# Performance work log

Measured on AMD Instinct MI355X. Metric: run time of the kernel, lower is better.

The kernel has to match this reference:

```python
import jax, jax.numpy as jnp
import numpy as np

GROUPS = 32  # min(32, 256//4)
EPS = 1e-5


def setup_inputs() -> dict:
    key = jax.random.key(0)
    ks = jax.random.split(key, 4)
    B, C, H, W = 8, 256, 128, 128
    x = jax.random.normal(ks[0], (B, C, H, W), dtype=jnp.float32)
    gn_w = jnp.ones((C,), dtype=jnp.float32)
    gn_b = jnp.zeros((C,), dtype=jnp.float32)
    qkv_w = jax.random.normal(ks[1], (3 * C, C), dtype=jnp.float32) * (C ** -0.5)
    qkv_b = jnp.zeros((3 * C,), dtype=jnp.float32)
    proj_w = jax.random.normal(ks[2], (C, C), dtype=jnp.float32) * (C ** -0.5)
    proj_b = jnp.zeros((C,), dtype=jnp.float32)
    return {"x": x, "gn_w": gn_w, "gn_b": gn_b, "qkv_w": qkv_w,
            "qkv_b": qkv_b, "proj_w": proj_w, "proj_b": proj_b}


def _group_norm(x, w, b):
    B, C, H, W = x.shape
    xg = x.reshape(B, GROUPS, C // GROUPS, H, W)
    mean = xg.mean(axis=(2, 3, 4), keepdims=True)
    var = xg.var(axis=(2, 3, 4), keepdims=True)
    xg = (xg - mean) * jax.lax.rsqrt(var + EPS)
    x = xg.reshape(B, C, H, W)
    return x * w[None, :, None, None] + b[None, :, None, None]


def reference(x, gn_w, gn_b, qkv_w, qkv_b, proj_w, proj_b):
    B, C, H, W = x.shape
    num_heads = 8
    head_dim = C // num_heads
    scale = head_dim ** -0.5

    h = _group_norm(x, gn_w, gn_b)
    # 1x1 conv == per-pixel matmul over channels
    qkv = jnp.einsum('bchw,oc->bohw', h, qkv_w) + qkv_b[None, :, None, None]
    qkv = qkv.reshape(B, 3, num_heads, head_dim, H * W)
    q, k, v = qkv[:, 0], qkv[:, 1], qkv[:, 2]  # each (B, h, head_dim, HW)
    # Faithful to source: contracts over spatial axis d=HW -> (B,h,hd,hd)
    attn = jnp.einsum('bhid,bhjd->bhij', q, k) * scale
    attn = jax.nn.softmax(attn, axis=-1)
    out = jnp.einsum('bhij,bhjd->bhid', attn, v)  # (B, h, head_dim, HW)
    out = out.reshape(B, C, H, W)
    out = jnp.einsum('bchw,oc->bohw', out, proj_w) + proj_b[None, :, None, None]
    return x + out
```

## Files before the change

### kernel.cpp

```cpp
#include <hip/hip_runtime.h>
#include <stdint.h>

typedef __bf16 bf16;
typedef __attribute__((ext_vector_type(8))) __bf16 bf16x8;
typedef __attribute__((ext_vector_type(4))) float f32x4;

#define S_HW 16384
#define N_C 256

__device__ __forceinline__ f32x4 mfma16(bf16x8 a, bf16x8 b, f32x4 c) {
  return __builtin_amdgcn_mfma_f32_16x16x32_bf16(a, b, c, 0, 0, 0);
}
__device__ __forceinline__ void async_ld16(const bf16* g, bf16* l) {
  __builtin_amdgcn_global_load_lds(
      (const __attribute__((address_space(1))) unsigned int*)g,
      (__attribute__((address_space(3))) unsigned int*)l, 16, 0, 0);
}
__device__ __forceinline__ unsigned short bf2u(bf16 h) {
  union { bf16 h; unsigned short u; } c; c.h = h; return c.u;
}
__device__ __forceinline__ bf16 u2bf(unsigned short u) {
  union { unsigned short u; bf16 h; } c; c.u = u; return c.h;
}

__global__ __launch_bounds__(256) void k_split(
    const float* __restrict__ x, bf16* __restrict__ yhi, bf16* __restrict__ ylo,
    bf16* __restrict__ yt, float* __restrict__ Sx) {
  int b = blockIdx.z, c0 = blockIdx.y * 64, s0 = blockIdx.x * 64;
  __shared__ unsigned T[64][65];
  __shared__ float sxl[256];
  int t = threadIdx.x;
  int cl = t >> 2, sg = t & 3;
  size_t off = (size_t)(b * N_C + c0 + cl) * S_HW + s0 + sg * 16;
  const float* xp = x + off;
  bf16x8 hv[2], lv[2];
  float sum = 0.f;
#pragma unroll
  for (int i2 = 0; i2 < 4; i2++) {
    float4 v = *(const float4*)(xp + i2 * 4);
    float f4[4] = {v.x, v.y, v.z, v.w};
#pragma unroll
    for (int k = 0; k < 4; k++) {
      int i = i2 * 4 + k;
      float fv = f4[k];
      bf16 h = (bf16)fv;
      bf16 l = (bf16)(fv - (float)h);
      hv[i >> 3][i & 7] = h;
      lv[i >> 3][i & 7] = l;
      sum += fv;
      T[sg * 16 + i][cl] = (unsigned)bf2u(h) | ((unsigned)bf2u(l) << 16);
    }
  }
  *(bf16x8*)(yhi + off) = hv[0];
  *(bf16x8*)(yhi + off + 8) = hv[1];
  *(bf16x8*)(ylo + off) = lv[0];
  *(bf16x8*)(ylo + off + 8) = lv[1];
  sxl[t] = sum;
  __syncthreads();
  if (t < 64) {
    float s2 = sxl[t * 4] + sxl[t * 4 + 1] + sxl[t * 4 + 2] + sxl[t * 4 + 3];
    atomicAdd(&Sx[b * N_C + c0 + t], s2);
  }
  int sl = t >> 2, cg = t & 3;
  bf16x8 ho[2], lo2[2];
#pragma unroll
  for (int i = 0; i < 16; i++) {
    unsigned u = T[sl][cg * 16 + i];
    ho[i >> 3][i & 7] = u2bf((unsigned short)(u & 0xffffu));
    lo2[i >> 3][i & 7] = u2bf((unsigned short)(u >> 16));
  }
  size_t tb = (size_t)(b * S_HW + s0 + sl) * 512 + c0 + cg * 16;
  *(bf16x8*)(yt + tb) = ho[0];
  *(bf16x8*)(yt + tb + 8) = ho[1];
  *(bf16x8*)(yt + tb + 256) = lo2[0];
  *(bf16x8*)(yt + tb + 256 + 8) = lo2[1];
}

__global__ __launch_bounds__(256) void k_gram(
    const bf16* __restrict__ yhi, const bf16* __restrict__ ylo,
    float* __restrict__ YG3) {
  constexpr int BK = 32;
  __shared__ __align__(16) bf16 As[128 * BK];
  __shared__ __align__(16) bf16 Bs[128 * BK];
  int kc = blockIdx.x * 2048;
  int m0 = (blockIdx.y >> 2) * 128, n0 = (blockIdx.y & 3) * 128;
  int b = blockIdx.z;
  int tid = threadIdx.x, lane = tid & 63, wave = tid >> 6;
  int wm = (wave >> 1) * 64, wn = (wave & 1) * 64;
  const bf16* Ab = yhi + (size_t)(b * N_C + m0) * S_HW;
  const bf16* Bb = (n0 < 256) ? yhi + (size_t)(b * N_C + n0) * S_HW
                              : ylo + (size_t)(b * N_C + n0 - 256) * S_HW;
  f32x4 acc[4][4] = {};
  for (int kt = kc; kt < kc + 2048; kt += BK) {
#pragma unroll
    for (int i = 0; i < 2; i++) {
      int ch = i * 256 + tid;
      int row = ch >> 2, col = (ch & 3) * 8;
      async_ld16(Ab + (size_t)row * S_HW + kt + col, As + (i * 256 + wave * 64) * 8);
      async_ld16(Bb + (size_t)row * S_HW + kt + col, Bs + (i * 256 + wave * 64) * 8);
    }
    __syncthreads();
    bf16x8 af[4], bfr[4];
    int fm = lane & 15, fk = (lane >> 4) * 8;
#pragma unroll
    for (int q = 0; q < 4; q++) {
      af[q] = *(const bf16x8*)(As + (wm + q * 16 + fm) * BK + fk);
      bfr[q] = *(const bf16x8*)(Bs + (wn + q * 16 + fm) * BK + fk);
    }
#pragma unroll
    for (int ti = 0; ti < 4; ti++)
#pragma unroll
      for (int tj = 0; tj < 4; tj++)
        acc[ti][tj] = mfma16(af[ti], bfr[tj], acc[ti][tj]);
    __syncthreads();
  }
  int quad = lane >> 4, cn = lane & 15;
#pragma unroll
  for (int ti = 0; ti < 4; ti++)
#pragma unroll
    for (int r = 0; r < 4; r++) {
      int m = m0 + wm + ti * 16 + quad * 4 + r;
#pragma unroll
      for (int tj = 0; tj < 4; tj++) {
        int n = n0 + wn + tj * 16 + cn;
        atomicAdd(&YG3[(size_t)(b * N_C + m) * 512 + n], acc[ti][tj][r]);
      }
    }
}

__global__ __launch_bounds__(256) void k_wkt(const float* __restrict__ qkv_w,
                                             float* __restrict__ WkT) {
  int k = blockIdx.x, j = threadIdx.x;
  WkT[k * 256 + j] = qkv_w[(256 + j) * 256 + k];
}

__global__ __launch_bounds__(256) void k_coefs(
    const float* __restrict__ Sx, const float* __restrict__ YG3,
    const float* __restrict__ gn_w, const float* __restrict__ gn_b,
    const float* __restrict__ qkv_w, const float* __restrict__ qkv_b,
    float* __restrict__ a_, float* __restrict__ bv_, float* __restrict__ u_,
    float* __restrict__ vbe) {
  int b = blockIdx.x, t = threadIdx.x;
  __shared__ float sxl[256], gxd[256], gm[32], gr[32], sh[256], bl[256];
  sxl[t] = Sx[b * N_C + t];
  gxd[t] = YG3[(size_t)(b * N_C + t) * 512 + t] +
           2.f * YG3[(size_t)(b * N_C + t) * 512 + 256 + t];
  __syncthreads();
  if (t < 32) {
    float s = 0.f, q2 = 0.f;
#pragma unroll
    for (int i = 0; i < 8; i++) { s += sxl[t * 8 + i]; q2 += gxd[t * 8 + i]; }
    float mean = s * (1.f / 131072.f);
    float var = q2 * (1.f / 131072.f) - mean * mean;
    gm[t] = mean;
    gr[t] = 1.f / sqrtf(var + 1e-5f);
  }
  __syncthreads();
  {
    float A = gn_w[t] * gr[t >> 3];
    float B = gn_b[t] - gm[t >> 3] * A;
    a_[b * N_C + t] = A;
    bv_[b * N_C + t] = B;
    bl[t] = B;
    sh[t] = A * sxl[t] + 16384.f * B;
  }
  __syncthreads();
  for (int r = t; r < 512; r += 256) {
    const float* wp = qkv_w + (size_t)r * 256;
    float acc = 0.f;
    for (int c = 0; c < 256; c++) acc += wp[c] * sh[c];
    u_[b * 512 + r] = acc;
  }
  {
    const float* wp = qkv_w + (size_t)(512 + t) * 256;
    float acc = 0.f;
    for (int c = 0; c < 256; c++) acc += wp[c] * bl[c];
    vbe[b * N_C + t] = acc + qkv_b[512 + t];
  }
}

__global__ __launch_bounds__(256) void k_t1(
    const float* __restrict__ YG3, const float* __restrict__ WkT,
    const float* __restrict__ a_, const float* __restrict__ bv_,
    const float* __restrict__ Sx, float* __restrict__ T1) {
  int tile = blockIdx.x, b = blockIdx.y;
  int i0 = (tile >> 2) * 64, j0 = (tile & 3) * 64;
  __shared__ float As[64][69];
  __shared__ float Bs[64][69];
  __shared__ float al[256], bl[256], sxl[256];
  int t = threadIdx.x;
  al[t] = a_[b * N_C + t];
  bl[t] = bv_[b * N_C + t];
  sxl[t] = Sx[b * N_C + t];
  int cl = t >> 2, qq = (t & 3) * 16;
  int kk = t >> 2, jj = (t & 3) * 16;
  int ti = t >> 4, tj = t & 15;
  float acc[4][4] = {};
  for (int kc = 0; kc < 256; kc += 64) {
    {
      const float* yg = YG3 + (size_t)(b * N_C + i0 + cl) * 512 + kc + qq;
#pragma unroll
      for (int i = 0; i < 16; i++) As[cl][qq + i] = yg[i] + yg[256 + i];
    }
    __syncthreads();
    {
      int cp = kc + kk;
      const float* ygp = YG3 + (size_t)(b * N_C + cp) * 512 + 256 + i0 + jj;
#pragma unroll
      for (int i = 0; i < 16; i++) As[jj + i][kk] += ygp[i];
    }
    __syncthreads();
    {
      int c = i0 + cl;
      float ac = al[c], bc = bl[c], sxc = sxl[c];
#pragma unroll
      for (int i = 0; i < 16; i++) {
        int cp = kc + qq + i;
        As[cl][qq + i] = ac * al[cp] * As[cl][qq + i] + ac * bl[cp] * sxc +
                         bc * al[cp] * sxl[cp] + 16384.f * bc * bl[cp];
      }
    }
    {
      const float* wp = WkT + (size_t)(kc + kk) * 256 + j0 + jj;
#pragma unroll
      for (int i = 0; i < 16; i += 4) {
        float4 v = *(const float4*)(wp + i);
        Bs[kk][jj + i] = v.x; Bs[kk][jj + i + 1] = v.y;
        Bs[kk][jj + i + 2] = v.z; Bs[kk][jj + i + 3] = v.w;
      }
    }
    __syncthreads();
    for (int k = 0; k < 64; k++) {
      float av[4], bv4[4];
#pragma unroll
      for (int ii = 0; ii < 4; ii++) av[ii] = As[ti * 4 + ii][k];
#pragma unroll
      for (int j2 = 0; j2 < 4; j2++) bv4[j2] = Bs[k][tj * 4 + j2];
#pragma unroll
      for (int ii = 0; ii < 4; ii++)
#pragma unroll
        for (int j2 = 0; j2 < 4; j2++) acc[ii][j2] += av[ii] * bv4[j2];
    }
    __syncthreads();
  }
#pragma unroll
  for (int ii = 0; ii < 4; ii++)
#pragma unroll
    for (int j2 = 0; j2 < 4; j2++)
      T1[(size_t)(b * N_C + i0 + ti * 4 + ii) * 256 + j0 + tj * 4 + j2] =
          acc[ii][j2];
}

__global__ __launch_bounds__(256) void k_logits(
    const float* __restrict__ T1, const float* __restrict__ qkv_w,
    const float* __restrict__ qkv_b, const float* __restrict__ u_,
    float* __restrict__ attn) {
  int h = blockIdx.x, b = blockIdx.y;
  __shared__ float Tc[64][33];
  __shared__ float Wql[32][65];
  __shared__ float Ll[32][33];
  __shared__ float uq[32], uk[32], bq[32], bk[32];
  int t = threadIdx.x;
  if (t < 32) {
    uq[t] = u_[b * 512 + h * 32 + t];
    uk[t] = u_[b * 512 + 256 + h * 32 + t];
    bq[t] = qkv_b[h * 32 + t];
    bk[t] = qkv_b[256 + h * 32 + t];
  }
  int i = t & 31, jg = t >> 5;
  float acc[4] = {};
  for (int cc = 0; cc < 256; cc += 64) {
    {
      int c_l = t >> 2, seg = (t & 3) * 8;
      const float* tp = T1 + (size_t)(b * N_C + cc + c_l) * 256 + h * 32 + seg;
      float4 v0 = *(const float4*)tp, v1 = *(const float4*)(tp + 4);
      Tc[c_l][seg] = v0.x; Tc[c_l][seg + 1] = v0.y;
      Tc[c_l][seg + 2] = v0.z; Tc[c_l][seg + 3] = v0.w;
      Tc[c_l][seg + 4] = v1.x; Tc[c_l][seg + 5] = v1.y;
      Tc[c_l][seg + 6] = v1.z; Tc[c_l][seg + 7] = v1.w;
      int row = t >> 3, seg2 = (t & 7) * 8;
      const float* wp = qkv_w + (size_t)(h * 32 + row) * 256 + cc + seg2;
      float4 w0 = *(const float4*)wp, w1 = *(const float4*)(wp + 4);
      Wql[row][seg2] = w0.x; Wql[row][seg2 + 1] = w0.y;
      Wql[row][seg2 + 2] = w0.z; Wql[row][seg2 + 3] = w0.w;
      Wql[row][seg2 + 4] = w1.x; Wql[row][seg2 + 5] = w1.y;
      Wql[row][seg2 + 6] = w1.z; Wql[row][seg2 + 7] = w1.w;
    }
    __syncthreads();
    for (int c = 0; c < 64; c++) {
      float w = Wql[i][c];
#pragma unroll
      for (int j2 = 0; j2 < 4; j2++) acc[j2] += w * Tc[c][jg * 4 + j2];
    }
    __syncthreads();
  }
  const float scale = 0.17677669529663687f;
#pragma unroll
  for (int j2 = 0; j2 < 4; j2++) {
    int j = jg * 4 + j2;
    Ll[i][j] = scale * (acc[j2] + bq[i] * uk[j] + bk[j] * uq[i] +
                        16384.f * bq[i] * bk[j]);
  }
  __syncthreads();
  if (t < 32) {
    float m = -1e30f;
    for (int j = 0; j < 32; j++) m = fmaxf(m, Ll[t][j]);
    float e[32], s = 0.f;
    for (int j = 0; j < 32; j++) { e[j] = expf(Ll[t][j] - m); s += e[j]; }
    float inv = 1.f / s;
    float* ap = attn + (size_t)((b * 8 + h) * 32 + t) * 32;
    for (int j = 0; j < 32; j++) ap[j] = e[j] * inv;
  }
}

__global__ __launch_bounds__(256) void k_m1(const float* __restrict__ proj_w,
                                            const float* __restrict__ attn,
                                            float* __restrict__ M1) {
  int o = blockIdx.x, b = blockIdx.y, t = threadIdx.x;
  __shared__ float at[8192];
  __shared__ float pl[256];
  for (int k = 0; k < 8192; k += 256) at[k + t] = attn[(size_t)b * 8192 + k + t];
  pl[t] = proj_w[(size_t)o * 256 + t];
  __syncthreads();
  int h = t >> 5, j = t & 31;
  float acc = 0.f;
#pragma unroll
  for (int i = 0; i < 32; i++) acc += pl[h * 32 + i] * at[h * 1024 + i * 32 + j];
  M1[(size_t)(b * N_C + o) * 256 + t] = acc;
}

__global__ __launch_bounds__(256) void k_m2(const float* __restrict__ M1,
                                            const float* __restrict__ qkv_w,
                                            float* __restrict__ M2) {
  int tile = blockIdx.x, b = blockIdx.y;
  int i0 = (tile >> 2) * 64, j0 = (tile & 3) * 64;
  __shared__ float As[64][69];
  __shared__ float Bs[64][69];
  int t = threadIdx.x;
  int cl = t >> 2, qq = (t & 3) * 16;
  int kk = t >> 2, jj = (t & 3) * 16;
  int ti = t >> 4, tj = t & 15;
  float acc[4][4] = {};
  for (int kc = 0; kc < 256; kc += 64) {
    {
      const float* mp = M1 + (size_t)(b * N_C + i0 + cl) * 256 + kc + qq;
#pragma unroll
      for (int i = 0; i < 16; i += 4) {
        float4 v = *(const float4*)(mp + i);
        As[cl][qq + i] = v.x; As[cl][qq + i + 1] = v.y;
        As[cl][qq + i + 2] = v.z; As[cl][qq + i + 3] = v.w;
      }
      const float* wp = qkv_w + (size_t)(512 + kc + kk) * 256 + j0 + jj;
#pragma unroll
      for (int i = 0; i < 16; i += 4) {
        float4 v = *(const float4*)(wp + i);
        Bs[kk][jj + i] = v.x; Bs[kk][jj + i + 1] = v.y;
        Bs[kk][jj + i + 2] = v.z; Bs[kk][jj + i + 3] = v.w;
      }
    }
    __syncthreads();
    for (int k = 0; k < 64; k++) {
      float av[4], bv4[4];
#pragma unroll
      for (int ii = 0; ii < 4; ii++) av[ii] = As[ti * 4 + ii][k];
#pragma unroll
      for (int j2 = 0; j2 < 4; j2++) bv4[j2] = Bs[k][tj * 4 + j2];
#pragma unroll
      for (int ii = 0; ii < 4; ii++)
#pragma unroll
        for (int j2 = 0; j2 < 4; j2++) acc[ii][j2] += av[ii] * bv4[j2];
    }
    __syncthreads();
  }
#pragma unroll
  for (int ii = 0; ii < 4; ii++)
#pragma unroll
    for (int j2 = 0; j2 < 4; j2++)
      M2[(size_t)(b * N_C + i0 + ti * 4 + ii) * 256 + j0 + tj * 4 + j2] =
          acc[ii][j2];
}

__global__ __launch_bounds__(256) void k_fa(
    const float* __restrict__ M2, const float* __restrict__ M1,
    const float* __restrict__ a_, const float* __restrict__ vbe,
    const float* __restrict__ proj_b, bf16* __restrict__ FA,
    float* __restrict__ g_) {
  int o = blockIdx.x, b = blockIdx.y, t = threadIdx.x;
  float f = M2[(size_t)(b * N_C + o) * 256 + t] * a_[b * N_C + t];
  bf16 hi = (bf16)f;
  bf16 lo = (bf16)(f - (float)hi);
  FA[(size_t)(b * N_C + o) * 512 + t] = hi;
  FA[(size_t)(b * N_C + o) * 512 + 256 + t] = lo;
  __shared__ float red[256];
  red[t] = M1[(size_t)(b * N_C + o) * 256 + t] * vbe[b * N_C + t];
  __syncthreads();
  for (int s2 = 128; s2 > 0; s2 >>= 1) {
    if (t < s2) red[t] += red[t + s2];
    __syncthreads();
  }
  if (t == 0) g_[b * N_C + o] = red[0] + proj_b[o];
}

__global__ __launch_bounds__(256) void k_final(
    const bf16* __restrict__ FA, const bf16* __restrict__ yt,
    const float* __restrict__ g_, const float* __restrict__ x,
    float* __restrict__ out) {
  constexpr int BK = 32;
  __shared__ __align__(16) bf16 As[128 * BK];
  __shared__ __align__(16) bf16 Bs[128 * BK];
  int b = blockIdx.z, m0 = blockIdx.y * 128, n0 = blockIdx.x * 128;
  int tid = threadIdx.x, lane = tid & 63, wave = tid >> 6;
  int wm = (wave >> 1) * 64, wn = (wave & 1) * 64;
  const bf16* Ab = FA + (size_t)(b * N_C + m0) * 512;
  const bf16* Bb = yt + (size_t)(b * S_HW + n0) * 512;
  f32x4 acc[4][4] = {};
  for (int kt = 0; kt < 768; kt += BK) {
    int ka = (kt < 512) ? kt : kt - 512;
    int kb = (kt < 256) ? kt : kt - 256;
#pragma unroll
    for (int i = 0; i < 2; i++) {
      int ch = i * 256 + tid;
      int row = ch >> 2, col = (ch & 3) * 8;
      async_ld16(Ab + (size_t)row * 512 + ka + col, As + (i * 256 + wave * 64) * 8);
      async_ld16(Bb + (size_t)row * 512 + kb + col, Bs + (i * 256 + wave * 64) * 8);
    }
    __syncthreads();
    bf16x8 af[4], bfr[4];
    int fm = lane & 15, fk = (lane >> 4) * 8;
#pragma unroll
    for (int q = 0; q < 4; q++) {
      af[q] = *(const bf16x8*)(As + (wm + q * 16 + fm) * BK + fk);
      bfr[q] = *(const bf16x8*)(Bs + (wn + q * 16 + fm) * BK + fk);
    }
#pragma unroll
    for (int ti = 0; ti < 4; ti++)
#pragma unroll
      for (int tj = 0; tj < 4; tj++)
        acc[ti][tj] = mfma16(af[ti], bfr[tj], acc[ti][tj]);
    __syncthreads();
  }
  int quad = lane >> 4, cn = lane & 15;
#pragma unroll
  for (int ti = 0; ti < 4; ti++)
#pragma unroll
    for (int r = 0; r < 4; r++) {
      int row = m0 + wm + ti * 16 + quad * 4 + r;
      float gb = g_[b * N_C + row];
#pragma unroll
      for (int tj = 0; tj < 4; tj++) {
        int col = n0 + wn + tj * 16 + cn;
        size_t idx = (size_t)(b * N_C + row) * S_HW + col;
        out[idx] = acc[ti][tj][r] + gb + x[idx];
      }
    }
}

extern "C" void kernel_launch(void* const* d_in, const int* in_sizes, int n_in,
                              void* d_out, int out_size, void* d_ws,
                              size_t ws_size, hipStream_t stream) {
  const float* x = (const float*)d_in[0];
  const float* gn_w = (const float*)d_in[1];
  const float* gn_b = (const float*)d_in[2];
  const float* qkv_w = (const float*)d_in[3];
  const float* qkv_b = (const float*)d_in[4];
  const float* proj_w = (const float*)d_in[5];
  const float* proj_b = (const float*)d_in[6];
  float* out = (float*)d_out;

  const size_t MB = 1ull << 20;
  char* ws = (char*)d_ws;
  bf16* ylo = (bf16*)ws;
  bf16* yt = (bf16*)(ws + 64 * MB);
  float* YG3 = (float*)(ws + 192 * MB);
  float* M1 = (float*)(ws + 192 * MB);
  bf16* FA = (bf16*)(ws + 194 * MB);
  float* WkT = (float*)(ws + 196 * MB);
  float* attn = (float*)(ws + 196 * MB + 256 * 1024);
  float* Sx = (float*)(ws + 196 * MB + 512 * 1024);
  float* a_ = (float*)(ws + 196 * MB + 520 * 1024);
  float* bv_ = (float*)(ws + 196 * MB + 528 * 1024);
  float* u_ = (float*)(ws + 196 * MB + 536 * 1024);
  float* vbe = (float*)(ws + 196 * MB + 552 * 1024);
  float* g_ = (float*)(ws + 196 * MB + 560 * 1024);
  float* T1 = (float*)(ws + 198 * MB);
  float* M2 = T1;
  bf16* yhi = (bf16*)d_out;

  if (ws_size < 200 * MB) return;

  hipMemsetAsync(YG3, 0, 4 * MB, stream);
  hipMemsetAsync(Sx, 0, 8 * 1024, stream);
  k_split<<<dim3(256, 4, 8), 256, 0, stream>>>(x, yhi, ylo, yt, Sx);
  k_gram<<<dim3(8, 8, 8), 256, 0, stream>>>(yhi, ylo, YG3);
  k_wkt<<<256, 256, 0, stream>>>(qkv_w, WkT);
  k_coefs<<<8, 256, 0, stream>>>(Sx, YG3, gn_w, gn_b, qkv_w, qkv_b, a_, bv_,
                                 u_, vbe);
  k_t1<<<dim3(16, 8), 256, 0, stream>>>(YG3, WkT, a_, bv_, Sx, T1);
  k_logits<<<dim3(8, 8), 256, 0, stream>>>(T1, qkv_w, qkv_b, u_, attn);
  k_m1<<<dim3(256, 8), 256, 0, stream>>>(proj_w, attn, M1);
  k_m2<<<dim3(16, 8), 256, 0, stream>>>(M1, qkv_w, M2);
  k_fa<<<dim3(256, 8), 256, 0, stream>>>(M2, M1, a_, vbe, proj_b, FA, g_);
  k_final<<<dim3(128, 2, 8), 256, 0, stream>>>(FA, yt, g_, x, out);
}
```

Before: 574.8 us.

## Fold residual into final GEMM via identity and double-buffer LDS tiles

The residual add x is folded into the final GEMM. k_fa adds 1.0 on the diagonal of FA, so the product with yt, which holds the bf16 hi/lo split of x, reproduces x. This drops the separate fp32 read of x in k_final's epilogue. Separately, k_gram and k_final get two LDS buffers per operand so the next K-tile is prefetched while the current one is consumed. The risks are slightly lower residual precision (a bf16 hi+lo reconstruction instead of exact fp32) and doubled LDS use per block, which may reduce occupancy.

```diff
diff --git a/kernel.cpp b/kernel.cpp
--- a/kernel.cpp
+++ b/kernel.cpp
@@ -80,8 +80,8 @@
     const bf16* __restrict__ yhi, const bf16* __restrict__ ylo,
     float* __restrict__ YG3) {
   constexpr int BK = 32;
-  __shared__ __align__(16) bf16 As[128 * BK];
-  __shared__ __align__(16) bf16 Bs[128 * BK];
+  __shared__ __align__(16) bf16 As[2][128 * BK];
+  __shared__ __align__(16) bf16 Bs[2][128 * BK];
   int kc = blockIdx.x * 2048;
   int m0 = (blockIdx.y >> 2) * 128, n0 = (blockIdx.y & 3) * 128;
   int b = blockIdx.z;
@@ -91,21 +91,30 @@
   const bf16* Bb = (n0 < 256) ? yhi + (size_t)(b * N_C + n0) * S_HW
                               : ylo + (size_t)(b * N_C + n0 - 256) * S_HW;
   f32x4 acc[4][4] = {};
-  for (int kt = kc; kt < kc + 2048; kt += BK) {
+
+  auto STAGE = [&](int buf, int kt) {
 #pragma unroll
     for (int i = 0; i < 2; i++) {
       int ch = i * 256 + tid;
       int row = ch >> 2, col = (ch & 3) * 8;
-      async_ld16(Ab + (size_t)row * S_HW + kt + col, As + (i * 256 + wave * 64) * 8);
-      async_ld16(Bb + (size_t)row * S_HW + kt + col, Bs + (i * 256 + wave * 64) * 8);
-    }
-    __syncthreads();
+      async_ld16(Ab + (size_t)row * S_HW + kt + col,
+                 &As[buf][(i * 256 + wave * 64) * 8]);
+      async_ld16(Bb + (size_t)row * S_HW + kt + col,
+                 &Bs[buf][(i * 256 + wave * 64) * 8]);
+    }
+  };
+
+  STAGE(0, kc);
+  __syncthreads();
+  int cur = 0;
+  for (int kt = kc; kt < kc + 2048; kt += BK) {
+    if (kt + BK < kc + 2048) STAGE(cur ^ 1, kt + BK);
     bf16x8 af[4], bfr[4];
     int fm = lane & 15, fk = (lane >> 4) * 8;
 #pragma unroll
     for (int q = 0; q < 4; q++) {
-      af[q] = *(const bf16x8*)(As + (wm + q * 16 + fm) * BK + fk);
-      bfr[q] = *(const bf16x8*)(Bs + (wn + q * 16 + fm) * BK + fk);
+      af[q] = *(const bf16x8*)(&As[cur][(wm + q * 16 + fm) * BK + fk]);
+      bfr[q] = *(const bf16x8*)(&Bs[cur][(wn + q * 16 + fm) * BK + fk]);
     }
 #pragma unroll
     for (int ti = 0; ti < 4; ti++)
@@ -113,6 +122,7 @@
       for (int tj = 0; tj < 4; tj++)
         acc[ti][tj] = mfma16(af[ti], bfr[tj], acc[ti][tj]);
     __syncthreads();
+    cur ^= 1;
   }
   int quad = lane >> 4, cn = lane & 15;
 #pragma unroll
@@ -386,7 +396,8 @@
     const float* __restrict__ proj_b, bf16* __restrict__ FA,
     float* __restrict__ g_) {
   int o = blockIdx.x, b = blockIdx.y, t = threadIdx.x;
-  float f = M2[(size_t)(b * N_C + o) * 256 + t] * a_[b * N_C + t];
+  float f = M2[(size_t)(b * N_C + o) * 256 + t] * a_[b * N_C + t] +
+            (t == o ? 1.0f : 0.0f);
   bf16 hi = (bf16)f;
   bf16 lo = (bf16)(f - (float)hi);
   FA[(size_t)(b * N_C + o) * 512 + t] = hi;
@@ -403,34 +414,42 @@
 
 __global__ __launch_bounds__(256) void k_final(
     const bf16* __restrict__ FA, const bf16* __restrict__ yt,
-    const float* __restrict__ g_, const float* __restrict__ x,
-    float* __restrict__ out) {
+    const float* __restrict__ g_, float* __restrict__ out) {
   constexpr int BK = 32;
-  __shared__ __align__(16) bf16 As[128 * BK];
-  __shared__ __align__(16) bf16 Bs[128 * BK];
+  __shared__ __align__(16) bf16 As[2][128 * BK];
+  __shared__ __align__(16) bf16 Bs[2][128 * BK];
   int b = blockIdx.z, m0 = blockIdx.y * 128, n0 = blockIdx.x * 128;
   int tid = threadIdx.x, lane = tid & 63, wave = tid >> 6;
   int wm = (wave >> 1) * 64, wn = (wave & 1) * 64;
   const bf16* Ab = FA + (size_t)(b * N_C + m0) * 512;
   const bf16* Bb = yt + (size_t)(b * S_HW + n0) * 512;
   f32x4 acc[4][4] = {};
-  for (int kt = 0; kt < 768; kt += BK) {
+
+  auto STAGE = [&](int buf, int kt) {
     int ka = (kt < 512) ? kt : kt - 512;
     int kb = (kt < 256) ? kt : kt - 256;
 #pragma unroll
     for (int i = 0; i < 2; i++) {
       int ch = i * 256 + tid;
       int row = ch >> 2, col = (ch & 3) * 8;
-      async_ld16(Ab + (size_t)row * 512 + ka + col, As + (i * 256 + wave * 64) * 8);
-      async_ld16(Bb + (size_t)row * 512 + kb + col, Bs + (i * 256 + wave * 64) * 8);
-    }
-    __syncthreads();
+      async_ld16(Ab + (size_t)row * 512 + ka + col,
+                 &As[buf][(i * 256 + wave * 64) * 8]);
+      async_ld16(Bb + (size_t)row * 512 + kb + col,
+                 &Bs[buf][(i * 256 + wave * 64) * 8]);
+    }
+  };
+
+  STAGE(0, 0);
+  __syncthreads();
+  int cur = 0;
+  for (int kt = 0; kt < 768; kt += BK) {
+    if (kt + BK < 768) STAGE(cur ^ 1, kt + BK);
     bf16x8 af[4], bfr[4];
     int fm = lane & 15, fk = (lane >> 4) * 8;
 #pragma unroll
     for (int q = 0; q < 4; q++) {
-      af[q] = *(const bf16x8*)(As + (wm + q * 16 + fm) * BK + fk);
-      bfr[q] = *(const bf16x8*)(Bs + (wn + q * 16 + fm) * BK + fk);
+      af[q] = *(const bf16x8*)(&As[cur][(wm + q * 16 + fm) * BK + fk]);
+      bfr[q] = *(const bf16x8*)(&Bs[cur][(wn + q * 16 + fm) * BK + fk]);
     }
 #pragma unroll
     for (int ti = 0; ti < 4; ti++)
@@ -438,6 +457,7 @@
       for (int tj = 0; tj < 4; tj++)
         acc[ti][tj] = mfma16(af[ti], bfr[tj], acc[ti][tj]);
     __syncthreads();
+    cur ^= 1;
   }
   int quad = lane >> 4, cn = lane & 15;
 #pragma unroll
@@ -450,7 +470,7 @@
       for (int tj = 0; tj < 4; tj++) {
         int col = n0 + wn + tj * 16 + cn;
         size_t idx = (size_t)(b * N_C + row) * S_HW + col;
-        out[idx] = acc[ti][tj][r] + gb + x[idx];
+        out[idx] = acc[ti][tj][r] + gb;
       }
     }
 }
@@ -500,5 +520,5 @@
   k_m1<<<dim3(256, 8), 256, 0, stream>>>(proj_w, attn, M1);
   k_m2<<<dim3(16, 8), 256, 0, stream>>>(M1, qkv_w, M2);
   k_fa<<<dim3(256, 8), 256, 0, stream>>>(M2, M1, a_, vbe, proj_b, FA, g_);
-  k_final<<<dim3(128, 2, 8), 256, 0, stream>>>(FA, yt, g_, x, out);
-}
+  k_final<<<dim3(128, 2, 8), 256, 0, stream>>>(FA, yt, g_, out);
+}
```

Measured after the change: 540.4 us. 6.0% less time.

## Fold residual into final GEMM via identity and drop LDS staging in GEMMs

Applied to the files above, without the earlier changes.

Adds an identity term to the FA coefficient matrix, so the final GEMM against the hi/lo split of x reproduces the residual add. This removes the separate fp32 read of x in the epilogue. The gram and final GEMM kernels also stop staging tiles in shared memory: fragments are loaded straight from global memory into registers, which removes the barriers. The trade-offs are that the residual is now rebuilt from the bf16 hi+lo split rather than exact fp32, and that operand reuse across waves now depends on the cache instead of LDS.

```diff
diff --git a/kernel.cpp b/kernel.cpp
--- a/kernel.cpp
+++ b/kernel.cpp
@@ -10,11 +10,6 @@
 
 __device__ __forceinline__ f32x4 mfma16(bf16x8 a, bf16x8 b, f32x4 c) {
   return __builtin_amdgcn_mfma_f32_16x16x32_bf16(a, b, c, 0, 0, 0);
-}
-__device__ __forceinline__ void async_ld16(const bf16* g, bf16* l) {
-  __builtin_amdgcn_global_load_lds(
-      (const __attribute__((address_space(1))) unsigned int*)g,
-      (__attribute__((address_space(3))) unsigned int*)l, 16, 0, 0);
 }
 __device__ __forceinline__ unsigned short bf2u(bf16 h) {
   union { bf16 h; unsigned short u; } c; c.h = h; return c.u;
@@ -79,9 +74,6 @@
 __global__ __launch_bounds__(256) void k_gram(
     const bf16* __restrict__ yhi, const bf16* __restrict__ ylo,
     float* __restrict__ YG3) {
-  constexpr int BK = 32;
-  __shared__ __align__(16) bf16 As[128 * BK];
-  __shared__ __align__(16) bf16 Bs[128 * BK];
   int kc = blockIdx.x * 2048;
   int m0 = (blockIdx.y >> 2) * 128, n0 = (blockIdx.y & 3) * 128;
   int b = blockIdx.z;
@@ -90,29 +82,22 @@
   const bf16* Ab = yhi + (size_t)(b * N_C + m0) * S_HW;
   const bf16* Bb = (n0 < 256) ? yhi + (size_t)(b * N_C + n0) * S_HW
                               : ylo + (size_t)(b * N_C + n0 - 256) * S_HW;
+  int fm = lane & 15, fk = (lane >> 4) * 8;
+  const bf16* Ap = Ab + (size_t)(wm + fm) * S_HW + kc + fk;
+  const bf16* Bp = Bb + (size_t)(wn + fm) * S_HW + kc + fk;
   f32x4 acc[4][4] = {};
-  for (int kt = kc; kt < kc + 2048; kt += BK) {
-#pragma unroll
-    for (int i = 0; i < 2; i++) {
-      int ch = i * 256 + tid;
-      int row = ch >> 2, col = (ch & 3) * 8;
-      async_ld16(Ab + (size_t)row * S_HW + kt + col, As + (i * 256 + wave * 64) * 8);
-      async_ld16(Bb + (size_t)row * S_HW + kt + col, Bs + (i * 256 + wave * 64) * 8);
-    }
-    __syncthreads();
+  for (int kt = 0; kt < 2048; kt += 32) {
     bf16x8 af[4], bfr[4];
-    int fm = lane & 15, fk = (lane >> 4) * 8;
 #pragma unroll
     for (int q = 0; q < 4; q++) {
-      af[q] = *(const bf16x8*)(As + (wm + q * 16 + fm) * BK + fk);
-      bfr[q] = *(const bf16x8*)(Bs + (wn + q * 16 + fm) * BK + fk);
+      af[q] = *(const bf16x8*)(Ap + (size_t)q * 16 * S_HW + kt);
+      bfr[q] = *(const bf16x8*)(Bp + (size_t)q * 16 * S_HW + kt);
     }
 #pragma unroll
     for (int ti = 0; ti < 4; ti++)
 #pragma unroll
       for (int tj = 0; tj < 4; tj++)
         acc[ti][tj] = mfma16(af[ti], bfr[tj], acc[ti][tj]);
-    __syncthreads();
   }
   int quad = lane >> 4, cn = lane & 15;
 #pragma unroll
@@ -386,7 +371,8 @@
     const float* __restrict__ proj_b, bf16* __restrict__ FA,
     float* __restrict__ g_) {
   int o = blockIdx.x, b = blockIdx.y, t = threadIdx.x;
-  float f = M2[(size_t)(b * N_C + o) * 256 + t] * a_[b * N_C + t];
+  float f = M2[(size_t)(b * N_C + o) * 256 + t] * a_[b * N_C + t] +
+            (t == o ? 1.0f : 0.0f);
   bf16 hi = (bf16)f;
   bf16 lo = (bf16)(f - (float)hi);
   FA[(size_t)(b * N_C + o) * 512 + t] = hi;
@@ -403,41 +389,28 @@
 
 __global__ __launch_bounds__(256) void k_final(
     const bf16* __restrict__ FA, const bf16* __restrict__ yt,
-    const float* __restrict__ g_, const float* __restrict__ x,
-    float* __restrict__ out) {
-  constexpr int BK = 32;
-  __shared__ __align__(16) bf16 As[128 * BK];
-  __shared__ __align__(16) bf16 Bs[128 * BK];
+    const float* __restrict__ g_, float* __restrict__ out) {
   int b = blockIdx.z, m0 = blockIdx.y * 128, n0 = blockIdx.x * 128;
   int tid = threadIdx.x, lane = tid & 63, wave = tid >> 6;
   int wm = (wave >> 1) * 64, wn = (wave & 1) * 64;
-  const bf16* Ab = FA + (size_t)(b * N_C + m0) * 512;
-  const bf16* Bb = yt + (size_t)(b * S_HW + n0) * 512;
+  int fm = lane & 15, fk = (lane >> 4) * 8;
+  const bf16* Ap = FA + (size_t)(b * N_C + m0 + wm + fm) * 512 + fk;
+  const bf16* Bp = yt + (size_t)(b * S_HW + n0 + wn + fm) * 512 + fk;
   f32x4 acc[4][4] = {};
-  for (int kt = 0; kt < 768; kt += BK) {
+  for (int kt = 0; kt < 768; kt += 32) {
     int ka = (kt < 512) ? kt : kt - 512;
     int kb = (kt < 256) ? kt : kt - 256;
-#pragma unroll
-    for (int i = 0; i < 2; i++) {
-      int ch = i * 256 + tid;
-      int row = ch >> 2, col = (ch & 3) * 8;
-      async_ld16(Ab + (size_t)row * 512 + ka + col, As + (i * 256 + wave * 64) * 8);
-      async_ld16(Bb + (size_t)row * 512 + kb + col, Bs + (i * 256 + wave * 64) * 8);
-    }
-    __syncthreads();
     bf16x8 af[4], bfr[4];
-    int fm = lane & 15, fk = (lane >> 4) * 8;
 #pragma unroll
     for (int q = 0; q < 4; q++) {
-      af[q] = *(const bf16x8*)(As + (wm + q * 16 + fm) * BK + fk);
-      bfr[q] = *(const bf16x8*)(Bs + (wn + q * 16 + fm) * BK + fk);
+      af[q] = *(const bf16x8*)(Ap + (size_t)q * 16 * 512 + ka);
+      bfr[q] = *(const bf16x8*)(Bp + (size_t)q * 16 * 512 + kb);
     }
 #pragma unroll
     for (int ti = 0; ti < 4; ti++)
 #pragma unroll
       for (int tj = 0; tj < 4; tj++)
         acc[ti][tj] = mfma16(af[ti], bfr[tj], acc[ti][tj]);
-    __syncthreads();
   }
   int quad = lane >> 4, cn = lane & 15;
 #pragma unroll
@@ -450,7 +423,7 @@
       for (int tj = 0; tj < 4; tj++) {
         int col = n0 + wn + tj * 16 + cn;
         size_t idx = (size_t)(b * N_C + row) * S_HW + col;
-        out[idx] = acc[ti][tj][r] + gb + x[idx];
+        out[idx] = acc[ti][tj][r] + gb;
       }
     }
 }
@@ -500,5 +473,5 @@
   k_m1<<<dim3(256, 8), 256, 0, stream>>>(proj_w, attn, M1);
   k_m2<<<dim3(16, 8), 256, 0, stream>>>(M1, qkv_w, M2);
   k_fa<<<dim3(256, 8), 256, 0, stream>>>(M2, M1, a_, vbe, proj_b, FA, g_);
-  k_final<<<dim3(128, 2, 8), 256, 0, stream>>>(FA, yt, g_, x, out);
-}
+  k_final<<<dim3(128, 2, 8), 256, 0, stream>>>(FA, yt, g_, out);
+}
```

After: 719.3 us. 25.1% more time.
